# Kernel optimization log

Measured on AMD Instinct MI355X. Metric: run time of the kernel, lower is better.

The kernel has to match this reference:

```python
import jax, jax.numpy as jnp
import numpy as np

T, I, H, C = 2048, 1024, 1024, 1000


def _lstm(x, W_ih, W_hh, b_ih, b_hh):
    # x: [T, I]; PyTorch LSTM gate order: i, f, g, o
    x_proj = x @ W_ih.T + b_ih + b_hh  # [T, 4H] input projection hoisted out of scan
    h_dim = W_hh.shape[1]

    def step(carry, xp):
        h, c = carry
        gates = xp + h @ W_hh.T  # [4H]
        i, f, g, o = jnp.split(gates, 4)
        i = jax.nn.sigmoid(i)
        f = jax.nn.sigmoid(f)
        g = jnp.tanh(g)
        o = jax.nn.sigmoid(o)
        c_new = f * c + i * g
        h_new = o * jnp.tanh(c_new)
        return (h_new, c_new), h_new

    h0 = jnp.zeros((h_dim,), x.dtype)
    (_, _), hs = jax.lax.scan(step, (h0, h0), x_proj)
    return hs  # [T, H]


def setup_inputs() -> dict:
    key = jax.random.key(0)
    ks = jax.random.split(key, 12)
    s = 1.0 / np.sqrt(H)  # torch LSTM uniform(-1/sqrt(H), 1/sqrt(H)) scale
    u = lambda k, shape: jax.random.uniform(k, shape, jnp.float32, -s, s)
    return {
        "x": jax.random.normal(ks[0], (T, I), jnp.float32),
        "W_ih_f": u(ks[1], (4 * H, I)),
        "W_hh_f": u(ks[2], (4 * H, H)),
        "b_ih_f": u(ks[3], (4 * H,)),
        "b_hh_f": u(ks[4], (4 * H,)),
        "W_ih_b": u(ks[5], (4 * H, I)),
        "W_hh_b": u(ks[6], (4 * H, H)),
        "b_ih_b": u(ks[7], (4 * H,)),
        "b_hh_b": u(ks[8], (4 * H,)),
        "fc_W": u(ks[9], (C, 2 * H)),
        "fc_b": u(ks[10], (C,)),
    }


def reference(x, W_ih_f, W_hh_f, b_ih_f, b_hh_f, W_ih_b, W_hh_b, b_ih_b, b_hh_b, fc_W, fc_b):
    h_fwd = _lstm(x, W_ih_f, W_hh_f, b_ih_f, b_hh_f)            # [T, H]
    h_bwd = _lstm(x[::-1], W_ih_b, W_hh_b, b_ih_b, b_hh_b)[::-1]  # [T, H], re-reversed
    h = jnp.concatenate([h_fwd, h_bwd], axis=-1)                  # [T, 2H]
    return h @ fc_W.T + fc_b                                      # [T, C]
```

## Files before the change

### kernel.cpp

```cpp
#include <hip/hip_runtime.h>
#include <hip/hip_bf16.h>
#include <cstdint>


typedef __fp16 h2 __attribute__((ext_vector_type(2)));
typedef __fp16 h8 __attribute__((ext_vector_type(8)));
typedef float f4 __attribute__((ext_vector_type(4)));
typedef unsigned long long u64;

#define T_LEN 2048

static __device__ __forceinline__ unsigned int packh2(float a, float b) {
  h2 r = __builtin_amdgcn_cvt_pkrtz(a, b);
  return __builtin_bit_cast(unsigned int, r);
}
static __device__ __forceinline__ float fdot2u(unsigned int a, unsigned int b, float c) {
  return __builtin_amdgcn_fdot2(__builtin_bit_cast(h2, a), __builtin_bit_cast(h2, b), c, false);
}
static __device__ __forceinline__ float sigmoidf_(float x) {
  return 1.f / (1.f + __expf(-x));
}
static __device__ __forceinline__ float tanhf_(float x) {
  float e = __expf(-2.f * fabsf(x));
  float r = (1.f - e) / (1.f + e);
  return copysignf(r, x);
}

__global__ void convert_all(const float* __restrict__ x, const float* __restrict__ wf,
                            const float* __restrict__ wb, const float* __restrict__ fcw,
                            _Float16* __restrict__ xf, _Float16* __restrict__ wff,
                            _Float16* __restrict__ wbf, _Float16* __restrict__ fcwf) {
  const size_t SX = 2097152, SW = 4194304, SFC = 2097152;
  size_t i = (size_t)blockIdx.x * 256 + threadIdx.x;
  if (i < SX) {
    xf[i] = (_Float16)x[i];
  } else if (i < SX + SW) {
    size_t j = i - SX; wff[j] = (_Float16)wf[j];
  } else if (i < SX + 2 * SW) {
    size_t j = i - SX - SW; wbf[j] = (_Float16)wb[j];
  } else if (i < SX + 2 * SW + SFC) {
    size_t j = i - SX - 2 * SW;
    int row = (int)(j >> 11), col = (int)(j & 2047);
    fcwf[j] = (row < 1000) ? (_Float16)fcw[(size_t)row * 2048 + col] : (_Float16)0.f;
  }
}

__global__ void init_state(u64* __restrict__ hc) {
  int t = threadIdx.x;
  for (int i = t; i < 2048; i += 256) hc[i] = 0ull;
}

#define LSTR 80

template <int MODE>
__global__ __launch_bounds__(256, 2) void gemm_f16(
    const _Float16* __restrict__ A, const _Float16* __restrict__ B,
    const float* __restrict__ bias1, const float* __restrict__ bias2,
    void* __restrict__ Cout, int M, int N, int K, int nout, int rev) {
  __shared__ _Float16 As[128 * LSTR];
  __shared__ _Float16 Bs[128 * LSTR];

  const int tid = threadIdx.x;
  const int ntn = N >> 7;
  const int tm = blockIdx.x / ntn, tn = blockIdx.x % ntn;
  const int wid = tid >> 6, lane = tid & 63;
  const int wr = wid >> 1, wc = wid & 1;
  const int quad = lane >> 4, l16 = lane & 15;

  const int srow = tid >> 1, seg = tid & 1;
  const int arow = rev ? (M - 1 - (tm * 128 + srow)) : (tm * 128 + srow);
  const int brow = tn * 128 + srow;

  f4 acc[4][4];
#pragma unroll
  for (int i = 0; i < 4; ++i)
#pragma unroll
    for (int j = 0; j < 4; ++j) acc[i][j] = (f4)0.f;

  for (int k0 = 0; k0 < K; k0 += 64) {
    uint4 va[4], vb[4];
    const uint4* gpa = (const uint4*)(A + (size_t)arow * K + k0 + seg * 32);
    const uint4* gpb = (const uint4*)(B + (size_t)brow * K + k0 + seg * 32);
#pragma unroll
    for (int c = 0; c < 4; ++c) va[c] = gpa[c];
#pragma unroll
    for (int c = 0; c < 4; ++c) vb[c] = gpb[c];

    __syncthreads();
    uint4* lpa = (uint4*)&As[srow * LSTR + seg * 32];
    uint4* lpb = (uint4*)&Bs[srow * LSTR + seg * 32];
#pragma unroll
    for (int c = 0; c < 4; ++c) lpa[c] = va[c];
#pragma unroll
    for (int c = 0; c < 4; ++c) lpb[c] = vb[c];
    __syncthreads();

#pragma unroll
    for (int kk = 0; kk < 64; kk += 32) {
      h8 af[4], bf[4];
#pragma unroll
      for (int i = 0; i < 4; ++i) {
        int m = wr * 64 + i * 16 + l16;
        af[i] = *(const h8*)&As[m * LSTR + kk + quad * 8];
        int n = wc * 64 + i * 16 + l16;
        bf[i] = *(const h8*)&Bs[n * LSTR + kk + quad * 8];
      }
#pragma unroll
      for (int i = 0; i < 4; ++i)
#pragma unroll
        for (int j = 0; j < 4; ++j)
          acc[i][j] = __builtin_amdgcn_mfma_f32_16x16x32_f16(af[i], bf[j], acc[i][j], 0, 0, 0);
    }
  }

  const int cm0 = tm * 128 + wr * 64, cn0 = tn * 128 + wc * 64;
#pragma unroll
  for (int i = 0; i < 4; ++i) {
#pragma unroll
    for (int j = 0; j < 4; ++j) {
      int n = cn0 + j * 16 + l16;
#pragma unroll
      for (int r = 0; r < 4; ++r) {
        int m = cm0 + i * 16 + quad * 4 + r;
        float v = acc[i][j][r];
        if (MODE == 0) {
          v += bias1[n] + bias2[n];
          ((_Float16*)Cout)[(size_t)m * N + n] = (_Float16)v;
        } else {
          if (n < nout) ((float*)Cout)[(size_t)m * nout + n] = v + bias1[n];
        }
      }
    }
  }
}

__global__ __launch_bounds__(256, 1) void lstm_rec(
    const float* __restrict__ Whh_f, const float* __restrict__ Whh_b,
    const _Float16* __restrict__ xp,
    u64* __restrict__ hc,
    _Float16* __restrict__ hhist) {
  const int tid = threadIdx.x;
  const int blk = blockIdx.x;
  const int dir = blk >> 6;
  const int ib = blk & 63;
  const int j0 = ib * 16;
  const int wv = tid >> 6;
  const int l = tid & 63;
  const int g = l >> 4;
  const int kq = l & 15;
  const int q = l & 3;
  const int wrow0 = g * 1024 + j0 + 4 * wv;

  const float* Whh = dir ? Whh_b : Whh_f;
  const _Float16* xpd = xp + (size_t)dir * (2048u * 4096u);

  __shared__ unsigned int lds_h[2][16 * 36];
  __shared__ float lds_tr[4 * 16];

  unsigned int w[4][32];
#pragma unroll
  for (int j = 0; j < 4; ++j) {
    const float* wp = Whh + (size_t)(wrow0 + j) * 1024 + kq * 64;
#pragma unroll
    for (int i = 0; i < 16; ++i) {
      float4 v = ((const float4*)wp)[i];
      w[j][2 * i] = packh2(v.x, v.y);
      w[j][2 * i + 1] = packh2(v.z, v.w);
    }
  }

  float c = 0.f;

  uint2 xv = *(const uint2*)(xpd + wrow0);
  h2 x01 = __builtin_bit_cast(h2, xv.x);
  h2 x23 = __builtin_bit_cast(h2, xv.y);
  float xf[4] = {(float)x01[0], (float)x01[1], (float)x23[0], (float)x23[1]};

  for (int t = 0; t < T_LEN; ++t) {
    const int buf = t & 1;
    unsigned d0, d1;
    {
      u64* src = hc + (((size_t)buf * 2 + dir) * 512 + 2 * tid);
      u64 a = __hip_atomic_load(&src[0], __ATOMIC_RELAXED, __HIP_MEMORY_SCOPE_AGENT);
      u64 b = __hip_atomic_load(&src[1], __ATOMIC_RELAXED, __HIP_MEMORY_SCOPE_AGENT);
      int cnt = 0;
      while ((unsigned)a != (unsigned)t || (unsigned)b != (unsigned)t) {
        if (++cnt > (1 << 12)) break;
        a = __hip_atomic_load(&src[0], __ATOMIC_RELAXED, __HIP_MEMORY_SCOPE_AGENT);
        b = __hip_atomic_load(&src[1], __ATOMIC_RELAXED, __HIP_MEMORY_SCOPE_AGENT);
      }
      d0 = (unsigned)(a >> 32);
      d1 = (unsigned)(b >> 32);
    }

    int tnx = (t + 1 < T_LEN) ? t + 1 : t;
    uint2 xn = *(const uint2*)(xpd + (size_t)tnx * 4096 + wrow0);

    *(uint2*)&lds_h[buf][(tid >> 4) * 36 + 2 * (tid & 15)] = make_uint2(d0, d1);
    __syncthreads();

    float acc0 = 0.f, acc1 = 0.f, acc2 = 0.f, acc3 = 0.f;
    const uint4* hp = (const uint4*)&lds_h[buf][kq * 36];
#pragma unroll
    for (int i = 0; i < 8; ++i) {
      uint4 hv = hp[i];
      acc0 = fdot2u(w[0][4 * i + 0], hv.x, acc0);
      acc0 = fdot2u(w[0][4 * i + 1], hv.y, acc0);
      acc0 = fdot2u(w[0][4 * i + 2], hv.z, acc0);
      acc0 = fdot2u(w[0][4 * i + 3], hv.w, acc0);
      acc1 = fdot2u(w[1][4 * i + 0], hv.x, acc1);
      acc1 = fdot2u(w[1][4 * i + 1], hv.y, acc1);
      acc1 = fdot2u(w[1][4 * i + 2], hv.z, acc1);
      acc1 = fdot2u(w[1][4 * i + 3], hv.w, acc1);
      acc2 = fdot2u(w[2][4 * i + 0], hv.x, acc2);
      acc2 = fdot2u(w[2][4 * i + 1], hv.y, acc2);
      acc2 = fdot2u(w[2][4 * i + 2], hv.z, acc2);
      acc2 = fdot2u(w[2][4 * i + 3], hv.w, acc2);
      acc3 = fdot2u(w[3][4 * i + 0], hv.x, acc3);
      acc3 = fdot2u(w[3][4 * i + 1], hv.y, acc3);
      acc3 = fdot2u(w[3][4 * i + 2], hv.z, acc3);
      acc3 = fdot2u(w[3][4 * i + 3], hv.w, acc3);
    }
#pragma unroll
    for (int m = 1; m < 16; m <<= 1) {
      acc0 += __shfl_xor(acc0, m, 64);
      acc1 += __shfl_xor(acc1, m, 64);
      acc2 += __shfl_xor(acc2, m, 64);
      acc3 += __shfl_xor(acc3, m, 64);
    }

    if (kq == 0) {
      f4 v = {acc0 + xf[0], acc1 + xf[1], acc2 + xf[2], acc3 + xf[3]};
      *(f4*)&lds_tr[wv * 16 + g * 4] = v;
    }
    float pi = lds_tr[wv * 16 + 0 + q];
    float pf = lds_tr[wv * 16 + 4 + q];
    float pg = lds_tr[wv * 16 + 8 + q];
    float po = lds_tr[wv * 16 + 12 + q];

    float ii = sigmoidf_(pi);
    float ff = sigmoidf_(pf);
    float g_ = tanhf_(pg);
    float oo = sigmoidf_(po);
    c = ff * c + ii * g_;
    float h = oo * tanhf_(c);

    float h1 = __shfl(h, 1, 64);
    float h2v = __shfl(h, 2, 64);
    float h3 = __shfl(h, 3, 64);
    if (l == 0) {
      unsigned p01 = packh2(h, h1);
      unsigned p23 = packh2(h2v, h3);
      u64 w0 = ((u64)p01 << 32) | (unsigned)(t + 1);
      u64 w1 = ((u64)p23 << 32) | (unsigned)(t + 1);
      u64* dst = hc + (((size_t)((t + 1) & 1) * 2 + dir) * 512 + (ib * 8 + 2 * wv));
      __hip_atomic_store(&dst[0], w0, __ATOMIC_RELAXED, __HIP_MEMORY_SCOPE_AGENT);
      __hip_atomic_store(&dst[1], w1, __ATOMIC_RELAXED, __HIP_MEMORY_SCOPE_AGENT);
      int tout = dir ? (T_LEN - 1 - t) : t;
      *(uint2*)&hhist[(size_t)tout * 2048 + dir * 1024 + j0 + 4 * wv] =
          make_uint2(p01, p23);
    }

    x01 = __builtin_bit_cast(h2, xn.x);
    x23 = __builtin_bit_cast(h2, xn.y);
    xf[0] = (float)x01[0]; xf[1] = (float)x01[1];
    xf[2] = (float)x23[0]; xf[3] = (float)x23[1];
  }
}

extern "C" void kernel_launch(void* const* d_in, const int* in_sizes, int n_in,
                              void* d_out, int out_size, void* d_ws, size_t ws_size,
                              hipStream_t stream) {
  (void)in_sizes; (void)n_in; (void)out_size; (void)ws_size;
  const float* x     = (const float*)d_in[0];
  const float* Wih_f = (const float*)d_in[1];
  const float* Whh_f = (const float*)d_in[2];
  const float* bih_f = (const float*)d_in[3];
  const float* bhh_f = (const float*)d_in[4];
  const float* Wih_b = (const float*)d_in[5];
  const float* Whh_b = (const float*)d_in[6];
  const float* bih_b = (const float*)d_in[7];
  const float* bhh_b = (const float*)d_in[8];
  const float* fcW   = (const float*)d_in[9];
  const float* fcb   = (const float*)d_in[10];

  char* ws = (char*)d_ws;
  _Float16* xf16   = (_Float16*)(ws + 0);
  _Float16* wih16f = (_Float16*)(ws + 4194304);
  _Float16* wih16b = (_Float16*)(ws + 12582912);
  _Float16* fcw16  = (_Float16*)(ws + 20971520);
  _Float16* xp16   = (_Float16*)(ws + 25165824);
  _Float16* hhist  = (_Float16*)(ws + 58720256);
  u64*      hc     = (u64*)     (ws + 67108864);

  const size_t SX = 2097152, SW = 4194304, SFC = 2097152;
  const size_t total_cvt = SX + 2 * SW + SFC;

  convert_all<<<dim3((unsigned)((total_cvt + 255) / 256)), 256, 0, stream>>>(
      x, Wih_f, Wih_b, fcW, xf16, wih16f, wih16b, fcw16);
  init_state<<<1, 256, 0, stream>>>(hc);

  gemm_f16<0><<<dim3(512), 256, 0, stream>>>(xf16, wih16f, bih_f, bhh_f,
                                             (void*)xp16, 2048, 4096, 1024, 4096, 0);
  gemm_f16<0><<<dim3(512), 256, 0, stream>>>(xf16, wih16b, bih_b, bhh_b,
                                             (void*)(xp16 + (size_t)2048 * 4096),
                                             2048, 4096, 1024, 4096, 1);

  lstm_rec<<<dim3(128), 256, 0, stream>>>(Whh_f, Whh_b, xp16, hc, hhist);

  gemm_f16<1><<<dim3(128), 256, 0, stream>>>(hhist, fcw16, fcb, nullptr,
                                             d_out, 2048, 1024, 2048, 1000, 0);
}
```

Measured before the change: 3.782 ms.

## Add fast sc0 polling path, epoch-tagged state, and spread recurrent blocks across XCDs

The per-step handoff of h between blocks now goes through a second buffer that is written with plain stores and polled with sc0 vector loads, which may hit a nearer cache level. The agent-scope atomic buffer is still written every step and checked every 16 polls as a fallback. An epoch counter tags the step values so stale data from earlier calls cannot match and no reset is needed between launches. The grid is widened to 512 blocks with most exiting at once, so the live blocks are spread across chiplets. The gate transpose now uses shuffles instead of LDS. This risks stale reads and only works if the hardware behaves as assumed.

Result: slower. 9.483 ms (+150.7%).

```diff
diff --git a/kernel.cpp b/kernel.cpp
--- a/kernel.cpp
+++ b/kernel.cpp
@@ -6,6 +6,7 @@
 typedef __fp16 h2 __attribute__((ext_vector_type(2)));
 typedef __fp16 h8 __attribute__((ext_vector_type(8)));
 typedef float f4 __attribute__((ext_vector_type(4)));
+typedef unsigned int u32x4 __attribute__((ext_vector_type(4)));
 typedef unsigned long long u64;
 
 #define T_LEN 2048
@@ -24,6 +25,18 @@
   float e = __expf(-2.f * fabsf(x));
   float r = (1.f - e) / (1.f + e);
   return copysignf(r, x);
+}
+
+static __device__ __forceinline__ void load4_sc0(const u64* p, u32x4& v) {
+  asm volatile(
+      "global_load_dwordx4 %0, %1, off sc0\n\t"
+      "s_waitcnt vmcnt(0)"
+      : "=&v"(v)
+      : "v"(p)
+      : "memory");
+}
+static __device__ __forceinline__ void store_u64_plain(u64* p, u64 v) {
+  asm volatile("global_store_dwordx2 %0, %1, off" :: "v"(p), "v"(v) : "memory");
 }
 
 __global__ void convert_all(const float* __restrict__ x, const float* __restrict__ wf,
@@ -45,9 +58,16 @@
   }
 }
 
-__global__ void init_state(u64* __restrict__ hc) {
-  int t = threadIdx.x;
-  for (int i = t; i < 2048; i += 256) hc[i] = 0ull;
+__global__ void init_state(u64* __restrict__ hc, u64* __restrict__ hcf,
+                           unsigned* __restrict__ ep) {
+  __shared__ unsigned sbs;
+  if (threadIdx.x == 0) sbs = atomicAdd(ep, 1u) << 12;
+  __syncthreads();
+  u64 v = (u64)sbs;
+  for (int i = threadIdx.x; i < 2048; i += 256) {
+    __hip_atomic_store(&hc[i], v, __ATOMIC_RELAXED, __HIP_MEMORY_SCOPE_AGENT);
+    __hip_atomic_store(&hcf[i], v, __ATOMIC_RELAXED, __HIP_MEMORY_SCOPE_AGENT);
+  }
 }
 
 #define LSTR 80
@@ -134,15 +154,18 @@
   }
 }
 
-__global__ __launch_bounds__(256, 1) void lstm_rec(
+__global__ __launch_bounds__(256, 2) void lstm_rec(
     const float* __restrict__ Whh_f, const float* __restrict__ Whh_b,
     const _Float16* __restrict__ xp,
     u64* __restrict__ hc,
+    u64* __restrict__ hcf,
+    unsigned* __restrict__ ep,
     _Float16* __restrict__ hhist) {
   const int tid = threadIdx.x;
   const int blk = blockIdx.x;
-  const int dir = blk >> 6;
-  const int ib = blk & 63;
+  const int dir = blk & 7;
+  if (dir > 1) return;
+  const int ib = blk >> 3;
   const int j0 = ib * 16;
   const int wv = tid >> 6;
   const int l = tid & 63;
@@ -151,11 +174,13 @@
   const int q = l & 3;
   const int wrow0 = g * 1024 + j0 + 4 * wv;
 
+  const unsigned SB =
+      (__hip_atomic_load(ep, __ATOMIC_RELAXED, __HIP_MEMORY_SCOPE_AGENT) - 1u) << 12;
+
   const float* Whh = dir ? Whh_b : Whh_f;
   const _Float16* xpd = xp + (size_t)dir * (2048u * 4096u);
 
   __shared__ unsigned int lds_h[2][16 * 36];
-  __shared__ float lds_tr[4 * 16];
 
   unsigned int w[4][32];
 #pragma unroll
@@ -178,19 +203,28 @@
 
   for (int t = 0; t < T_LEN; ++t) {
     const int buf = t & 1;
-    unsigned d0, d1;
+    const unsigned exp0 = SB + (unsigned)t;
+    unsigned d0 = 0, d1 = 0;
     {
-      u64* src = hc + (((size_t)buf * 2 + dir) * 512 + 2 * tid);
-      u64 a = __hip_atomic_load(&src[0], __ATOMIC_RELAXED, __HIP_MEMORY_SCOPE_AGENT);
-      u64 b = __hip_atomic_load(&src[1], __ATOMIC_RELAXED, __HIP_MEMORY_SCOPE_AGENT);
+      const size_t boff = ((size_t)buf * 2 + dir) * 512 + 2 * tid;
+      const u64* f = hcf + boff;
+      u64* s = hc + boff;
       int cnt = 0;
-      while ((unsigned)a != (unsigned)t || (unsigned)b != (unsigned)t) {
-        if (++cnt > (1 << 12)) break;
-        a = __hip_atomic_load(&src[0], __ATOMIC_RELAXED, __HIP_MEMORY_SCOPE_AGENT);
-        b = __hip_atomic_load(&src[1], __ATOMIC_RELAXED, __HIP_MEMORY_SCOPE_AGENT);
+      for (;;) {
+        u32x4 fv;
+        load4_sc0(f, fv);
+        if (fv[0] == exp0 && fv[2] == exp0) { d0 = fv[1]; d1 = fv[3]; break; }
+        if ((++cnt & 15) == 0) {
+          u64 sa = __hip_atomic_load(&s[0], __ATOMIC_RELAXED, __HIP_MEMORY_SCOPE_AGENT);
+          u64 sb = __hip_atomic_load(&s[1], __ATOMIC_RELAXED, __HIP_MEMORY_SCOPE_AGENT);
+          if ((unsigned)sa == exp0 && (unsigned)sb == exp0) {
+            d0 = (unsigned)(sa >> 32);
+            d1 = (unsigned)(sb >> 32);
+            break;
+          }
+          if (cnt > (1 << 12)) break;
+        }
       }
-      d0 = (unsigned)(a >> 32);
-      d1 = (unsigned)(b >> 32);
     }
 
     int tnx = (t + 1 < T_LEN) ? t + 1 : t;
@@ -229,14 +263,12 @@
       acc3 += __shfl_xor(acc3, m, 64);
     }
 
-    if (kq == 0) {
-      f4 v = {acc0 + xf[0], acc1 + xf[1], acc2 + xf[2], acc3 + xf[3]};
-      *(f4*)&lds_tr[wv * 16 + g * 4] = v;
-    }
-    float pi = lds_tr[wv * 16 + 0 + q];
-    float pf = lds_tr[wv * 16 + 4 + q];
-    float pg = lds_tr[wv * 16 + 8 + q];
-    float po = lds_tr[wv * 16 + 12 + q];
+    float av = (q == 0) ? (acc0 + xf[0]) : (q == 1) ? (acc1 + xf[1])
+             : (q == 2) ? (acc2 + xf[2]) : (acc3 + xf[3]);
+    float pi = __shfl(av, q, 64);
+    float pf = __shfl(av, 16 + q, 64);
+    float pg = __shfl(av, 32 + q, 64);
+    float po = __shfl(av, 48 + q, 64);
 
     float ii = sigmoidf_(pi);
     float ff = sigmoidf_(pf);
@@ -245,20 +277,17 @@
     c = ff * c + ii * g_;
     float h = oo * tanhf_(c);
 
-    float h1 = __shfl(h, 1, 64);
-    float h2v = __shfl(h, 2, 64);
-    float h3 = __shfl(h, 3, 64);
-    if (l == 0) {
-      unsigned p01 = packh2(h, h1);
-      unsigned p23 = packh2(h2v, h3);
-      u64 w0 = ((u64)p01 << 32) | (unsigned)(t + 1);
-      u64 w1 = ((u64)p23 << 32) | (unsigned)(t + 1);
-      u64* dst = hc + (((size_t)((t + 1) & 1) * 2 + dir) * 512 + (ib * 8 + 2 * wv));
-      __hip_atomic_store(&dst[0], w0, __ATOMIC_RELAXED, __HIP_MEMORY_SCOPE_AGENT);
-      __hip_atomic_store(&dst[1], w1, __ATOMIC_RELAXED, __HIP_MEMORY_SCOPE_AGENT);
+    float hx = __shfl_xor(h, 1, 64);
+    if (l < 4 && (l & 1) == 0) {
+      unsigned pk = packh2(h, hx);
+      u64 wv64 = ((u64)pk << 32) | (u64)(SB + (unsigned)(t + 1));
+      size_t widx = ((size_t)((t + 1) & 1) * 2 + dir) * 512 +
+                    (size_t)(ib * 8 + 2 * wv + (l >> 1));
+      store_u64_plain(hcf + widx, wv64);
+      __hip_atomic_store(&hc[widx], wv64, __ATOMIC_RELAXED, __HIP_MEMORY_SCOPE_AGENT);
       int tout = dir ? (T_LEN - 1 - t) : t;
-      *(uint2*)&hhist[(size_t)tout * 2048 + dir * 1024 + j0 + 4 * wv] =
-          make_uint2(p01, p23);
+      *(unsigned*)&hhist[(size_t)tout * 2048 +
+                         (size_t)(dir * 1024 + j0 + 4 * wv + (l >> 1) * 2)] = pk;
     }
 
     x01 = __builtin_bit_cast(h2, xn.x);
@@ -292,13 +321,15 @@
   _Float16* xp16   = (_Float16*)(ws + 25165824);
   _Float16* hhist  = (_Float16*)(ws + 58720256);
   u64*      hc     = (u64*)     (ws + 67108864);
+  u64*      hcf    = (u64*)     (ws + 67125248);
+  unsigned* epoch  = (unsigned*)(ws + 67141632);
 
   const size_t SX = 2097152, SW = 4194304, SFC = 2097152;
   const size_t total_cvt = SX + 2 * SW + SFC;
 
   convert_all<<<dim3((unsigned)((total_cvt + 255) / 256)), 256, 0, stream>>>(
       x, Wih_f, Wih_b, fcW, xf16, wih16f, wih16b, fcw16);
-  init_state<<<1, 256, 0, stream>>>(hc);
+  init_state<<<1, 256, 0, stream>>>(hc, hcf, epoch);
 
   gemm_f16<0><<<dim3(512), 256, 0, stream>>>(xf16, wih16f, bih_f, bhh_f,
                                              (void*)xp16, 2048, 4096, 1024, 4096, 0);
@@ -306,7 +337,7 @@
                                              (void*)(xp16 + (size_t)2048 * 4096),
                                              2048, 4096, 1024, 4096, 1);
 
-  lstm_rec<<<dim3(128), 256, 0, stream>>>(Whh_f, Whh_b, xp16, hc, hhist);
+  lstm_rec<<<dim3(512), 256, 0, stream>>>(Whh_f, Whh_b, xp16, hc, hcf, epoch, hhist);
 
   gemm_f16<1><<<dim3(128), 256, 0, stream>>>(hhist, fcw16, fcb, nullptr,
                                              d_out, 2048, 1024, 2048, 1000, 0);
```
